# Optimization experiments

Measured on AMD Instinct MI355X. Metric: run time of the kernel, lower is better.

The kernel has to match this reference:

```python
import jax, jax.numpy as jnp
import numpy as np

RADII = (0.8, 1.6)
NSAMPLES = (16, 32)
NUM_GRIDPOINTS = 216


def rotate_z(points, theta):
    # points (b, n, m, 3), theta (b, n); rotate xy about z-axis
    c = jnp.cos(theta)[:, :, None]
    s = jnp.sin(theta)[:, :, None]
    x, y, z = points[..., 0], points[..., 1], points[..., 2]
    return jnp.stack([c * x - s * y, s * x + c * y, z], axis=-1)


def ball_query(d2, radius, nsample):
    # d2: (b, Ng, K) squared distances. Returns first nsample in-radius point
    # indices per query (CUDA ball_query semantics: pad with first found index,
    # 0 if none found).
    K = d2.shape[-1]
    ar = jnp.arange(K, dtype=jnp.int32)
    scores = jnp.where(d2 < radius * radius, ar, K)  # K == sentinel for 'not in ball'
    idx = -jax.lax.top_k(-scores, nsample)[0]        # nsample smallest => first hits, ascending
    first = idx[..., :1]
    idx = jnp.where(idx >= K, first, idx)
    idx = jnp.where(idx >= K, 0, idx)
    return idx


def gather_group(xyz, feats_t, new_xyz, idx):
    # xyz (b,K,3), feats_t (b,K,C), new_xyz (b,Ng,3), idx (b,Ng,ns)
    gx = jax.vmap(lambda p, i: p[i])(xyz, idx)      # (b,Ng,ns,3)
    gf = jax.vmap(lambda f, i: f[i])(feats_t, idx)  # (b,Ng,ns,C)
    rel = gx - new_xyz[:, :, None, :]               # use_xyz=True relative coords
    return jnp.concatenate([rel, gf], axis=-1)      # (b,Ng,ns,3+C)


def setup_inputs() -> dict:
    key = jax.random.key(0)
    ks = jax.random.split(key, 12)
    b, n, m, K, C = 2, 48, NUM_GRIDPOINTS, 2048, 128
    proposals = jax.random.uniform(ks[0], (b, n, 7), dtype=jnp.float32)
    keypoint_xyz = jax.random.normal(ks[1], (b, K, 3), dtype=jnp.float32)
    keypoint_features = jax.random.normal(ks[2], (b, C, K), dtype=jnp.float32)
    grid_noise = jax.random.uniform(ks[3], (b, n, m, 3), dtype=jnp.float32)

    def lin(k, o, i):
        return jax.random.normal(k, (o, i), dtype=jnp.float32) / np.float32(np.sqrt(i))

    w0_0 = lin(ks[4], 64, C + 3)
    w0_1 = lin(ks[5], 64, 64)
    w1_0 = lin(ks[6], 64, C + 3)
    w1_1 = lin(ks[7], 64, 64)
    red_w0 = lin(ks[8], 256, 128 * m)
    red_w1 = lin(ks[9], 256, 256)
    z64 = jnp.zeros((64,), jnp.float32)
    return {
        'proposals': proposals, 'keypoint_xyz': keypoint_xyz,
        'keypoint_features': keypoint_features, 'grid_noise': grid_noise,
        'w0_0': w0_0, 'b0_0': z64, 'w0_1': w0_1, 'b0_1': z64,
        'w1_0': w1_0, 'b1_0': z64, 'w1_1': w1_1, 'b1_1': z64,
        'red_w0': red_w0, 'red_b0': jnp.zeros((256,), jnp.float32),
        'red_w1': red_w1, 'red_b1': jnp.zeros((256,), jnp.float32),
    }


def reference(proposals, keypoint_xyz, keypoint_features, grid_noise,
              w0_0, b0_0, w0_1, b0_1, w1_0, b1_0, w1_1, b1_1,
              red_w0, red_b0, red_w1, red_b1):
    b, n, _ = proposals.shape
    m = NUM_GRIDPOINTS
    # sample_gridpoints: uniform in box dims, rotate by yaw, shift to center
    grid = grid_noise * proposals[:, :, None, 3:6]
    grid = rotate_z(grid, proposals[..., 6]) + proposals[:, :, None, 0:3]
    new_xyz = grid.reshape(b, n * m, 3)                      # (b, Ng, 3)
    # squared pairwise distances via |a|^2 + |b|^2 - 2ab (avoids (b,Ng,K,3) temp)
    d2 = (jnp.sum(new_xyz * new_xyz, -1)[:, :, None]
          + jnp.sum(keypoint_xyz * keypoint_xyz, -1)[:, None, :]
          - 2.0 * jnp.einsum('bnd,bkd->bnk', new_xyz, keypoint_xyz))
    feats_t = jnp.transpose(keypoint_features, (0, 2, 1))    # (b, K, C)
    scale_params = [((w0_0, b0_0), (w0_1, b0_1)), ((w1_0, b1_0), (w1_1, b1_1))]
    outs = []
    for radius, ns, layers in zip(RADII, NSAMPLES, scale_params):
        idx = ball_query(d2, radius, ns)                     # (b, Ng, ns)
        x = gather_group(keypoint_xyz, feats_t, new_xyz, idx)  # (b, Ng, ns, 3+C)
        for W, bias in layers:                               # shared 1x1-conv MLP (BN folded)
            x = jax.nn.relu(jnp.einsum('bnsc,oc->bnso', x, W) + bias)
        outs.append(jnp.max(x, axis=2))                      # max-pool over neighbors
    x = jnp.concatenate(outs, axis=-1)                       # (b, Ng, Cout)
    Cout = x.shape[-1]
    # (b, Cout, n, m).permute(0,2,1,3).view(b, n, Cout*m) equivalent
    x = x.reshape(b, n, m, Cout).transpose(0, 1, 3, 2).reshape(b, n, Cout * m)
    x = jax.nn.relu(x @ red_w0.T + red_b0)
    x = jax.nn.relu(x @ red_w1.T + red_b1)
    return x
```

## Files before the change

### kernel.cpp

```cpp
#include <hip/hip_runtime.h>
#include <cstdint>

#define NPROP  48
#define MGRID  216
#define NPT    (NPROP*MGRID)
#define KPT    2048
#define CFEAT  128
#define R0SQ   0.64f
#define R1SQ   2.56f
#define NS0    16
#define NS1    32
#define KRED   (CFEAT*MGRID)
#define NPOINTS (2*NPT)
#define NKSPLIT 108

typedef float f32x4  __attribute__((ext_vector_type(4)));
typedef short bf16x8 __attribute__((ext_vector_type(8)));
typedef unsigned long long ull;

#define AFRAG_OFF 0
#define KX4_OFF   8192
#define Q0_OFF    24576
#define POOL_OFF  548864
#define PT_OFF    3203072
#define PART_OFF  5857280

__device__ __forceinline__ unsigned short bf_rne(float x) {
    unsigned u = __float_as_uint(x);
    return (unsigned short)((u + 0x7fffu + ((u >> 16) & 1u)) >> 16);
}
__device__ __forceinline__ float bf_f32(unsigned short h) {
    return __uint_as_float(((unsigned)h) << 16);
}

__global__ __launch_bounds__(64) void k_pre(
    const float* __restrict__ kxyz,
    const float* __restrict__ w01, const float* __restrict__ w11,
    float* __restrict__ ws)
{
    int bid = blockIdx.x;
    if (bid < 16) {
        int kc = bid & 1, ot = (bid >> 1) & 3, s = bid >> 3;
        const float* W = s ? w11 : w01;
        int l   = threadIdx.x;
        int row = ot*16 + (l & 15);
        int k0  = kc*32 + (l >> 4)*8;
        union { unsigned short u16[8]; bf16x8 v; } hh, hl;
#pragma unroll
        for (int j = 0; j < 8; ++j) {
            float x  = W[row*64 + k0 + j];
            unsigned short hi = bf_rne(x);
            hh.u16[j] = hi;
            hl.u16[j] = bf_rne(x - bf_f32(hi));
        }
        bf16x8* Ahi = (bf16x8*)(ws + AFRAG_OFF);
        bf16x8* Alo = Ahi + 16*64;
        int fi = (s*4 + ot)*2 + kc;
        Ahi[fi*64 + l] = hh.v;
        Alo[fi*64 + l] = hl.v;
    } else {
        int idx = (bid - 16)*64 + threadIdx.x;
        const float* kp = kxyz + (size_t)idx*3;
        float kx = kp[0], ky = kp[1], kz = kp[2];
        float kn2 = fmaf(kz, kz, fmaf(ky, ky, kx*kx));
        f32x4 v = {kx, ky, kz, kn2};
        ((f32x4*)(ws + KX4_OFF))[idx] = v;
    }
}

__global__ __launch_bounds__(256) void k_qproj(
    const float* __restrict__ kxyz, const float* __restrict__ feats,
    const float* __restrict__ w0, const float* __restrict__ b0,
    const float* __restrict__ w1, const float* __restrict__ b1,
    float* __restrict__ ws)
{
    __shared__ float wl[64*131];
    int bid  = blockIdx.x;
    int kgrp = bid & 511;
    int s    = (bid >> 9) & 1;
    int b    = bid >> 10;
    const float* W    = s ? w1 : w0;
    const float* bias = s ? b1 : b0;
    for (int i = threadIdx.x; i < 64*131; i += 256) wl[i] = W[i];
    __syncthreads();
    int k = kgrp*4 + (threadIdx.x >> 6);
    int o = threadIdx.x & 63;
    float acc = bias[o];
    const float* kp = kxyz + ((size_t)b*KPT + k)*3;
    acc = fmaf(wl[o*131+0], kp[0], acc);
    acc = fmaf(wl[o*131+1], kp[1], acc);
    acc = fmaf(wl[o*131+2], kp[2], acc);
    const float* f = feats + (size_t)b*CFEAT*KPT + k;
#pragma unroll 8
    for (int c = 0; c < CFEAT; ++c)
        acc = fmaf(wl[o*131+3+c], f[(size_t)c*KPT], acc);
    ws[Q0_OFF + (size_t)s*(2*KPT*64) + ((size_t)b*KPT + k)*64 + o] = acc;
}

template <int NST>
__device__ __forceinline__ void build_bfrag(
    const float* __restrict__ Qb, const int* __restrict__ idxl,
    const float* __restrict__ u_lds,
    bf16x8 (&Bhi)[NST][2], bf16x8 (&Blo)[NST][2], int lane)
{
    const int g = lane >> 4;
#pragma unroll
    for (int st = 0; st < NST; ++st) {
        int sp = idxl[st*16 + (lane & 15)];
        const float* qr = Qb + ((size_t)sp << 6) + g*8;
#pragma unroll
        for (int kc = 0; kc < 2; ++kc) {
            f32x4 q0 = *(const f32x4*)(qr + kc*32);
            f32x4 q1 = *(const f32x4*)(qr + kc*32 + 4);
            f32x4 u0 = *(const f32x4*)(u_lds + kc*32 + g*8);
            f32x4 u1 = *(const f32x4*)(u_lds + kc*32 + g*8 + 4);
            union { unsigned short u16[8]; bf16x8 v; } hh, hl;
#pragma unroll
            for (int j = 0; j < 4; ++j) {
                float x = fmaxf(q0[j] - u0[j], 0.f);
                unsigned short hi = bf_rne(x);
                hh.u16[j] = hi;
                hl.u16[j] = bf_rne(x - bf_f32(hi));
                float y = fmaxf(q1[j] - u1[j], 0.f);
                unsigned short hi2 = bf_rne(y);
                hh.u16[j+4] = hi2;
                hl.u16[j+4] = bf_rne(y - bf_f32(hi2));
            }
            Bhi[st][kc] = hh.v;
            Blo[st][kc] = hl.v;
        }
    }
}

template <int NST>
__device__ __forceinline__ void mfma_eval(
    const bf16x8* Ahi, const bf16x8* Alo,
    const float* __restrict__ bs,
    const bf16x8 (&Bhi)[NST][2], const bf16x8 (&Blo)[NST][2],
    float* stage, int sbase, int lane)
{
    const int g = lane >> 4;
#pragma unroll
    for (int ot = 0; ot < 4; ++ot) {
        int fi = (sbase + ot)*2;
        bf16x8 ah0 = Ahi[(fi+0)*64 + lane];
        bf16x8 ah1 = Ahi[(fi+1)*64 + lane];
        bf16x8 al0 = Alo[(fi+0)*64 + lane];
        bf16x8 al1 = Alo[(fi+1)*64 + lane];
        f32x4 bv = *(const f32x4*)(bs + ot*16 + g*4);
        f32x4 rmax = {0.f, 0.f, 0.f, 0.f};
#pragma unroll
        for (int st = 0; st < NST; ++st) {
            f32x4 acc = {0.f, 0.f, 0.f, 0.f};
            acc = __builtin_amdgcn_mfma_f32_16x16x32_bf16(al0, Bhi[st][0], acc, 0,0,0);
            acc = __builtin_amdgcn_mfma_f32_16x16x32_bf16(al1, Bhi[st][1], acc, 0,0,0);
            acc = __builtin_amdgcn_mfma_f32_16x16x32_bf16(ah0, Blo[st][0], acc, 0,0,0);
            acc = __builtin_amdgcn_mfma_f32_16x16x32_bf16(ah1, Blo[st][1], acc, 0,0,0);
            acc = __builtin_amdgcn_mfma_f32_16x16x32_bf16(ah0, Bhi[st][0], acc, 0,0,0);
            acc = __builtin_amdgcn_mfma_f32_16x16x32_bf16(ah1, Bhi[st][1], acc, 0,0,0);
#pragma unroll
            for (int r = 0; r < 4; ++r)
                rmax[r] = fmaxf(rmax[r], fmaxf(acc[r] + bv[r], 0.f));
        }
#pragma unroll
        for (int m = 1; m < 16; m <<= 1) {
#pragma unroll
            for (int r = 0; r < 4; ++r)
                rmax[r] = fmaxf(rmax[r], __shfl_xor(rmax[r], m));
        }
        if ((lane & 15) == 0)
            *(f32x4*)(stage + ot*16 + g*4) = rmax;
    }
}

__global__ __launch_bounds__(256) void k_main(
    const float* __restrict__ proposals, const float* __restrict__ grid_noise,
    const float* __restrict__ w00, const float* __restrict__ b01,
    const float* __restrict__ w10, const float* __restrict__ b11,
    float* __restrict__ ws)
{
    __shared__ __align__(16) float afrag[8192];
    __shared__ int idx0s[4][NS0];
    __shared__ int idx1s[4][NS1];
    __shared__ __align__(16) float u0l[4][64], u1l[4][64];
    __shared__ __align__(16) float stage[4][64];
    const int wid  = threadIdx.x >> 6;
    const int lane = threadIdx.x & 63;

    {
        const f32x4* src = (const f32x4*)(ws + AFRAG_OFF);
        f32x4* dst = (f32x4*)afrag;
        for (int t = threadIdx.x; t < 2048; t += 256) dst[t] = src[t];
    }
    __syncthreads();

    const int p = blockIdx.x*4 + wid;
    int b   = p / NPT;
    int rem = p - b*NPT;
    int i   = rem / MGRID;
    int g   = rem - i*MGRID;

    float a0x = w00[lane*131+0], a0y = w00[lane*131+1], a0z = w00[lane*131+2];
    float a1x = w10[lane*131+0], a1y = w10[lane*131+1], a1z = w10[lane*131+2];

    const float* pr = proposals  + ((size_t)b*NPROP + i)*7;
    const float* gn = grid_noise + (((size_t)b*NPROP + i)*MGRID + g)*3;
    float gx = gn[0]*pr[3], gy = gn[1]*pr[4], gz = gn[2]*pr[5];
    float th = pr[6];
    float ss = sinf(th), cc = cosf(th);
    float nx = cc*gx - ss*gy + pr[0];
    float ny = ss*gx + cc*gy + pr[1];
    float nz = gz + pr[2];
    float pn2 = nx*nx + ny*ny + nz*nz;
    u0l[wid][lane] = a0x*nx + a0y*ny + a0z*nz;
    u1l[wid][lane] = a1x*nx + a1y*ny + a1z*nz;

    int* idx0 = idx0s[wid];
    int* idx1 = idx1s[wid];
    int cnt0 = 0, cnt1 = 0;
    const f32x4* kx4 = (const f32x4*)(ws + KX4_OFF) + (size_t)b*KPT;
    ull ltm = (1ull << lane) - 1ull;

#define BQ_PROC(D2, RSQ, KK, CNT, IDX, NSV)                                   \
    {                                                                         \
        ull m = __ballot((D2) < RSQ);                                         \
        if (m) {                                                              \
            int pre = __popcll(m & ltm);                                      \
            if (((m >> lane) & 1ull) && CNT + pre < NSV) IDX[CNT + pre] = (KK);\
            CNT += __popcll(m);                                               \
        }                                                                     \
    }

    for (int ck = 0; ck < KPT/64; ck += 2) {
        f32x4 ka  = kx4[ck*64 + lane];
        f32x4 kc2 = kx4[ck*64 + 64 + lane];
        float dta = fmaf(nz, ka.z, fmaf(ny, ka.y, nx*ka.x));
        float d2a = fmaf(-2.f, dta, pn2 + ka.w);
        float dtb = fmaf(nz, kc2.z, fmaf(ny, kc2.y, nx*kc2.x));
        float d2b = fmaf(-2.f, dtb, pn2 + kc2.w);
        int kka = ck*64 + lane, kkb = kka + 64;
        if (cnt0 < NS0) {
            BQ_PROC(d2a, R0SQ, kka, cnt0, idx0, NS0)
            BQ_PROC(d2b, R0SQ, kkb, cnt0, idx0, NS0)
        }
        if (cnt1 < NS1) {
            BQ_PROC(d2a, R1SQ, kka, cnt1, idx1, NS1)
            BQ_PROC(d2b, R1SQ, kkb, cnt1, idx1, NS1)
        }
        if (cnt0 >= NS0 && cnt1 >= NS1) break;
    }
#undef BQ_PROC

    if (lane == 0) {
        if (cnt0 == 0) idx0[0] = 0;
        if (cnt1 == 0) idx1[0] = 0;
    }
    asm volatile("s_waitcnt lgkmcnt(0)" ::: "memory");
    __builtin_amdgcn_wave_barrier();
    int na0 = cnt0 ? min(cnt0, NS0) : 1;
    int na1 = cnt1 ? min(cnt1, NS1) : 1;
    int f0 = idx0[0], f1 = idx1[0];
    if (lane >= na0 && lane < NS0) idx0[lane] = f0;
    if (lane >= na1 && lane < NS1) idx1[lane] = f1;
    asm volatile("s_waitcnt lgkmcnt(0)" ::: "memory");
    __builtin_amdgcn_wave_barrier();

    const float*  Qb0 = ws + Q0_OFF + (size_t)b*(KPT*64);
    const float*  Qb1 = ws + Q0_OFF + (size_t)(2*KPT*64) + (size_t)b*(KPT*64);
    const bf16x8* Ahi = (const bf16x8*)afrag;
    const bf16x8* Alo = Ahi + 16*64;

    bf16x8 B0hi[1][2], B0lo[1][2], B1hi[2][2], B1lo[2][2];
    build_bfrag<1>(Qb0, idx0, u0l[wid], B0hi, B0lo, lane);
    build_bfrag<2>(Qb1, idx1, u1l[wid], B1hi, B1lo, lane);

    mfma_eval<1>(Ahi, Alo, b01, B0hi, B0lo, stage[wid], 0, lane);
    asm volatile("s_waitcnt lgkmcnt(0)" ::: "memory");
    __builtin_amdgcn_wave_barrier();
    float mx0 = stage[wid][lane];
    __builtin_amdgcn_wave_barrier();

    mfma_eval<2>(Ahi, Alo, b11, B1hi, B1lo, stage[wid], 4, lane);
    asm volatile("s_waitcnt lgkmcnt(0)" ::: "memory");
    __builtin_amdgcn_wave_barrier();
    float mx1 = stage[wid][lane];

    ws[POOL_OFF + (size_t)p*CFEAT + lane]      = mx0;
    ws[POOL_OFF + (size_t)p*CFEAT + 64 + lane] = mx1;
}

template <int W>
__device__ __forceinline__ void ptr_tile(const float* __restrict__ in,
                                         float* __restrict__ out,
                                         float* __restrict__ t, int g0)
{
    for (int idx = threadIdx.x; idx < 128*W; idx += 256) {
        int gg = idx >> 7, c = idx & 127;
        t[c*(W+1) + gg] = in[(size_t)(g0+gg)*128 + c];
    }
    __syncthreads();
    for (int idx = threadIdx.x; idx < 128*W; idx += 256) {
        int c = idx / W, gg = idx - c*W;
        out[c*216 + g0 + gg] = t[c*(W+1) + gg];
    }
}

__global__ __launch_bounds__(256) void k_ptr(float* __restrict__ ws)
{
    __shared__ float t[128*33];
    int bid = blockIdx.x;
    int row = bid / 7, tt = bid - row*7;
    const float* in = ws + POOL_OFF + (size_t)row*MGRID*CFEAT;
    float* out = ws + PT_OFF + (size_t)row*KRED;
    if (tt < 6) ptr_tile<32>(in, out, t, tt*32);
    else        ptr_tile<24>(in, out, t, 192);
}

__global__ __launch_bounds__(256) void k_red0(
    const float* __restrict__ A, const float* __restrict__ w0,
    float* __restrict__ part)
{
    __shared__ __align__(16) float Al[96*68];
    __shared__ __align__(16) float Bl[64*68];
    int bid = blockIdx.x;
    int ot  = bid & 3;
    int ks  = bid >> 2;
    int tid = threadIdx.x;
    int tx  = tid & 15, ty = tid >> 4;
    float acc[6][4] = {};

    for (int chunk = 0; chunk < 4; ++chunk) {
        int kk0 = ks*256 + chunk*64;
#pragma unroll
        for (int j = 0; j < 6; ++j) {
            int f4i = tid + j*256;
            int rr = f4i >> 4, c4 = f4i & 15;
            float4 v = *(const float4*)(A + (size_t)rr*KRED + kk0 + c4*4);
            *(float4*)(Al + rr*68 + c4*4) = v;
        }
#pragma unroll
        for (int j = 0; j < 4; ++j) {
            int f4i = tid + j*256;
            int rr = f4i >> 4, c4 = f4i & 15;
            float4 v = *(const float4*)(w0 + (size_t)(ot*64+rr)*KRED + kk0 + c4*4);
            *(float4*)(Bl + rr*68 + c4*4) = v;
        }
        __syncthreads();
#pragma unroll
        for (int k4 = 0; k4 < 16; ++k4) {
            float4 av[6], bv[4];
#pragma unroll
            for (int q = 0; q < 6; ++q) av[q] = *(const float4*)(Al + (ty*6+q)*68 + k4*4);
#pragma unroll
            for (int u = 0; u < 4; ++u) bv[u] = *(const float4*)(Bl + (u*16+tx)*68 + k4*4);
#pragma unroll
            for (int q = 0; q < 6; ++q)
#pragma unroll
                for (int u = 0; u < 4; ++u) {
                    acc[q][u] = fmaf(av[q].x, bv[u].x, acc[q][u]);
                    acc[q][u] = fmaf(av[q].y, bv[u].y, acc[q][u]);
                    acc[q][u] = fmaf(av[q].z, bv[u].z, acc[q][u]);
                    acc[q][u] = fmaf(av[q].w, bv[u].w, acc[q][u]);
                }
        }
        __syncthreads();
    }
    float* pp = part + (size_t)ks*(96*256);
#pragma unroll
    for (int q = 0; q < 6; ++q)
#pragma unroll
        for (int u = 0; u < 4; ++u)
            pp[(size_t)(ty*6+q)*256 + ot*64 + u*16 + tx] = acc[q][u];
}

__global__ __launch_bounds__(256) void k_fin(
    const float* __restrict__ part, const float* __restrict__ rb0,
    const float* __restrict__ w1, const float* __restrict__ rb1,
    float* __restrict__ out)
{
    __shared__ __align__(16) float hbuf[256];
    int r = blockIdx.x, o = threadIdx.x;
    const float* pp = part + (size_t)r*256 + o;
    float s0 = 0.f, s1 = 0.f, s2 = 0.f, s3 = 0.f;
#pragma unroll 4
    for (int ks = 0; ks < NKSPLIT; ks += 4) {
        s0 += pp[(size_t)(ks+0)*(96*256)];
        s1 += pp[(size_t)(ks+1)*(96*256)];
        s2 += pp[(size_t)(ks+2)*(96*256)];
        s3 += pp[(size_t)(ks+3)*(96*256)];
    }
    float h = fmaxf(((s0 + s1) + (s2 + s3)) + rb0[o], 0.f);
    hbuf[o] = h;
    __syncthreads();
    float a0 = rb1[o], a1 = 0.f, a2 = 0.f, a3 = 0.f;
    const float4* wrow = (const float4*)(w1 + (size_t)o*256);
    const float4* hv   = (const float4*)hbuf;
#pragma unroll 8
    for (int j = 0; j < 64; ++j) {
        float4 w = wrow[j], x = hv[j];
        a0 = fmaf(w.x, x.x, a0);
        a1 = fmaf(w.y, x.y, a1);
        a2 = fmaf(w.z, x.z, a2);
        a3 = fmaf(w.w, x.w, a3);
    }
    out[(size_t)r*256 + o] = fmaxf((a0 + a1) + (a2 + a3), 0.f);
}

extern "C" void kernel_launch(void* const* d_in, const int* in_sizes, int n_in,
                              void* d_out, int out_size, void* d_ws, size_t ws_size,
                              hipStream_t stream)
{
    (void)in_sizes; (void)n_in; (void)out_size; (void)ws_size;
    const float* proposals = (const float*)d_in[0];
    const float* kxyz      = (const float*)d_in[1];
    const float* feats     = (const float*)d_in[2];
    const float* gnoise    = (const float*)d_in[3];
    const float* w0_0 = (const float*)d_in[4];
    const float* b0_0 = (const float*)d_in[5];
    const float* w0_1 = (const float*)d_in[6];
    const float* b0_1 = (const float*)d_in[7];
    const float* w1_0 = (const float*)d_in[8];
    const float* b1_0 = (const float*)d_in[9];
    const float* w1_1 = (const float*)d_in[10];
    const float* b1_1 = (const float*)d_in[11];
    const float* rw0  = (const float*)d_in[12];
    const float* rb0  = (const float*)d_in[13];
    const float* rw1  = (const float*)d_in[14];
    const float* rb1  = (const float*)d_in[15];
    float* ws  = (float*)d_ws;
    float* out = (float*)d_out;

    k_pre  <<<  80,  64, 0, stream>>>(kxyz, w0_1, w1_1, ws);
    k_qproj<<<2048, 256, 0, stream>>>(kxyz, feats, w0_0, b0_0, w1_0, b1_0, ws);
    k_main <<<5184, 256, 0, stream>>>(proposals, gnoise,
                                      w0_0, b0_1, w1_0, b1_1, ws);
    k_ptr  <<< 672, 256, 0, stream>>>(ws);
    k_red0 <<< 432, 256, 0, stream>>>(ws + PT_OFF, rw0, ws + PART_OFF);
    k_fin  <<<  96, 256, 0, stream>>>(ws + PART_OFF, rb0, rw1, rb1, out);
}
```

Before: 247.6 us.

## Transpose MFMA operands in k_main to pool in registers and double block size

Swaps the MFMA operand roles so the gathered hidden activations form the row operand and the weights the column operand. The max-pool over neighbors then needs only two cross-lane shuffles per output tile, and the result is chosen per lane with selects instead of a 16-lane shuffle tree plus an LDS staging round-trip. k_main also moves to 512-thread blocks (8 waves, launch bounds 512,6), so the weight-fragment LDS copy is amortised over twice as many points. The larger blocks and the occupancy hint may raise register pressure or limit occupancy.

```diff
diff --git a/kernel.cpp b/kernel.cpp
--- a/kernel.cpp
+++ b/kernel.cpp
@@ -53,11 +53,11 @@
             hh.u16[j] = hi;
             hl.u16[j] = bf_rne(x - bf_f32(hi));
         }
-        bf16x8* Ahi = (bf16x8*)(ws + AFRAG_OFF);
-        bf16x8* Alo = Ahi + 16*64;
+        bf16x8* Whi = (bf16x8*)(ws + AFRAG_OFF);
+        bf16x8* Wlo = Whi + 16*64;
         int fi = (s*4 + ot)*2 + kc;
-        Ahi[fi*64 + l] = hh.v;
-        Alo[fi*64 + l] = hl.v;
+        Whi[fi*64 + l] = hh.v;
+        Wlo[fi*64 + l] = hl.v;
     } else {
         int idx = (bid - 16)*64 + threadIdx.x;
         const float* kp = kxyz + (size_t)idx*3;
@@ -98,10 +98,10 @@
 }
 
 template <int NST>
-__device__ __forceinline__ void build_bfrag(
+__device__ __forceinline__ void build_hfrag(
     const float* __restrict__ Qb, const int* __restrict__ idxl,
     const float* __restrict__ u_lds,
-    bf16x8 (&Bhi)[NST][2], bf16x8 (&Blo)[NST][2], int lane)
+    bf16x8 (&Hhi)[NST][2], bf16x8 (&Hlo)[NST][2], int lane)
 {
     const int g = lane >> 4;
 #pragma unroll
@@ -126,75 +126,75 @@
                 hh.u16[j+4] = hi2;
                 hl.u16[j+4] = bf_rne(y - bf_f32(hi2));
             }
-            Bhi[st][kc] = hh.v;
-            Blo[st][kc] = hl.v;
+            Hhi[st][kc] = hh.v;
+            Hlo[st][kc] = hl.v;
         }
     }
 }
 
 template <int NST>
-__device__ __forceinline__ void mfma_eval(
-    const bf16x8* Ahi, const bf16x8* Alo,
+__device__ __forceinline__ float eval_T(
+    const bf16x8* Whi, const bf16x8* Wlo,
     const float* __restrict__ bs,
-    const bf16x8 (&Bhi)[NST][2], const bf16x8 (&Blo)[NST][2],
-    float* stage, int sbase, int lane)
-{
-    const int g = lane >> 4;
-#pragma unroll
-    for (int ot = 0; ot < 4; ++ot) {
-        int fi = (sbase + ot)*2;
-        bf16x8 ah0 = Ahi[(fi+0)*64 + lane];
-        bf16x8 ah1 = Ahi[(fi+1)*64 + lane];
-        bf16x8 al0 = Alo[(fi+0)*64 + lane];
-        bf16x8 al1 = Alo[(fi+1)*64 + lane];
-        f32x4 bv = *(const f32x4*)(bs + ot*16 + g*4);
-        f32x4 rmax = {0.f, 0.f, 0.f, 0.f};
-#pragma unroll
-        for (int st = 0; st < NST; ++st) {
-            f32x4 acc = {0.f, 0.f, 0.f, 0.f};
-            acc = __builtin_amdgcn_mfma_f32_16x16x32_bf16(al0, Bhi[st][0], acc, 0,0,0);
-            acc = __builtin_amdgcn_mfma_f32_16x16x32_bf16(al1, Bhi[st][1], acc, 0,0,0);
-            acc = __builtin_amdgcn_mfma_f32_16x16x32_bf16(ah0, Blo[st][0], acc, 0,0,0);
-            acc = __builtin_amdgcn_mfma_f32_16x16x32_bf16(ah1, Blo[st][1], acc, 0,0,0);
-            acc = __builtin_amdgcn_mfma_f32_16x16x32_bf16(ah0, Bhi[st][0], acc, 0,0,0);
-            acc = __builtin_amdgcn_mfma_f32_16x16x32_bf16(ah1, Bhi[st][1], acc, 0,0,0);
-#pragma unroll
-            for (int r = 0; r < 4; ++r)
-                rmax[r] = fmaxf(rmax[r], fmaxf(acc[r] + bv[r], 0.f));
-        }
-#pragma unroll
-        for (int m = 1; m < 16; m <<= 1) {
-#pragma unroll
-            for (int r = 0; r < 4; ++r)
-                rmax[r] = fmaxf(rmax[r], __shfl_xor(rmax[r], m));
-        }
-        if ((lane & 15) == 0)
-            *(f32x4*)(stage + ot*16 + g*4) = rmax;
-    }
-}
-
-__global__ __launch_bounds__(256) void k_main(
+    const bf16x8 (&Hhi)[NST][2], const bf16x8 (&Hlo)[NST][2],
+    int sbase, int lane)
+{
+    float r0, r1, r2, r3;
+#define EVAL_OT(OT, ROUT)                                                     \
+    {                                                                         \
+        int fi = (sbase + (OT))*2;                                            \
+        bf16x8 wh0 = Whi[(fi+0)*64 + lane];                                   \
+        bf16x8 wh1 = Whi[(fi+1)*64 + lane];                                   \
+        bf16x8 wl0 = Wlo[(fi+0)*64 + lane];                                   \
+        bf16x8 wl1 = Wlo[(fi+1)*64 + lane];                                   \
+        float bc = bs[(OT)*16 + (lane & 15)];                                 \
+        f32x4 rmax = {0.f, 0.f, 0.f, 0.f};                                    \
+        _Pragma("unroll")                                                     \
+        for (int st = 0; st < NST; ++st) {                                    \
+            f32x4 acc = {0.f, 0.f, 0.f, 0.f};                                 \
+            acc = __builtin_amdgcn_mfma_f32_16x16x32_bf16(Hlo[st][0], wh0, acc, 0,0,0); \
+            acc = __builtin_amdgcn_mfma_f32_16x16x32_bf16(Hlo[st][1], wh1, acc, 0,0,0); \
+            acc = __builtin_amdgcn_mfma_f32_16x16x32_bf16(Hhi[st][0], wl0, acc, 0,0,0); \
+            acc = __builtin_amdgcn_mfma_f32_16x16x32_bf16(Hhi[st][1], wl1, acc, 0,0,0); \
+            acc = __builtin_amdgcn_mfma_f32_16x16x32_bf16(Hhi[st][0], wh0, acc, 0,0,0); \
+            acc = __builtin_amdgcn_mfma_f32_16x16x32_bf16(Hhi[st][1], wh1, acc, 0,0,0); \
+            _Pragma("unroll")                                                 \
+            for (int r = 0; r < 4; ++r)                                       \
+                rmax[r] = fmaxf(rmax[r], fmaxf(acc[r] + bc, 0.f));            \
+        }                                                                     \
+        float mm = fmaxf(fmaxf(rmax[0], rmax[1]), fmaxf(rmax[2], rmax[3]));   \
+        mm = fmaxf(mm, __shfl_xor(mm, 16));                                   \
+        mm = fmaxf(mm, __shfl_xor(mm, 32));                                   \
+        ROUT = mm;                                                            \
+    }
+    EVAL_OT(0, r0) EVAL_OT(1, r1) EVAL_OT(2, r2) EVAL_OT(3, r3)
+#undef EVAL_OT
+    float v01 = (lane & 16) ? r1 : r0;
+    float v23 = (lane & 16) ? r3 : r2;
+    return (lane & 32) ? v23 : v01;
+}
+
+__global__ __launch_bounds__(512, 6) void k_main(
     const float* __restrict__ proposals, const float* __restrict__ grid_noise,
     const float* __restrict__ w00, const float* __restrict__ b01,
     const float* __restrict__ w10, const float* __restrict__ b11,
     float* __restrict__ ws)
 {
     __shared__ __align__(16) float afrag[8192];
-    __shared__ int idx0s[4][NS0];
-    __shared__ int idx1s[4][NS1];
-    __shared__ __align__(16) float u0l[4][64], u1l[4][64];
-    __shared__ __align__(16) float stage[4][64];
+    __shared__ int idx0s[8][NS0];
+    __shared__ int idx1s[8][NS1];
+    __shared__ __align__(16) float u0l[8][64], u1l[8][64];
     const int wid  = threadIdx.x >> 6;
     const int lane = threadIdx.x & 63;
 
     {
         const f32x4* src = (const f32x4*)(ws + AFRAG_OFF);
         f32x4* dst = (f32x4*)afrag;
-        for (int t = threadIdx.x; t < 2048; t += 256) dst[t] = src[t];
+        for (int t = threadIdx.x; t < 2048; t += 512) dst[t] = src[t];
     }
     __syncthreads();
 
-    const int p = blockIdx.x*4 + wid;
+    const int p = blockIdx.x*8 + wid;
     int b   = p / NPT;
     int rem = p - b*NPT;
     int i   = rem / MGRID;
@@ -267,23 +267,15 @@
 
     const float*  Qb0 = ws + Q0_OFF + (size_t)b*(KPT*64);
     const float*  Qb1 = ws + Q0_OFF + (size_t)(2*KPT*64) + (size_t)b*(KPT*64);
-    const bf16x8* Ahi = (const bf16x8*)afrag;
-    const bf16x8* Alo = Ahi + 16*64;
-
-    bf16x8 B0hi[1][2], B0lo[1][2], B1hi[2][2], B1lo[2][2];
-    build_bfrag<1>(Qb0, idx0, u0l[wid], B0hi, B0lo, lane);
-    build_bfrag<2>(Qb1, idx1, u1l[wid], B1hi, B1lo, lane);
-
-    mfma_eval<1>(Ahi, Alo, b01, B0hi, B0lo, stage[wid], 0, lane);
-    asm volatile("s_waitcnt lgkmcnt(0)" ::: "memory");
-    __builtin_amdgcn_wave_barrier();
-    float mx0 = stage[wid][lane];
-    __builtin_amdgcn_wave_barrier();
-
-    mfma_eval<2>(Ahi, Alo, b11, B1hi, B1lo, stage[wid], 4, lane);
-    asm volatile("s_waitcnt lgkmcnt(0)" ::: "memory");
-    __builtin_amdgcn_wave_barrier();
-    float mx1 = stage[wid][lane];
+    const bf16x8* Whi = (const bf16x8*)afrag;
+    const bf16x8* Wlo = Whi + 16*64;
+
+    bf16x8 H0hi[1][2], H0lo[1][2], H1hi[2][2], H1lo[2][2];
+    build_hfrag<1>(Qb0, idx0, u0l[wid], H0hi, H0lo, lane);
+    build_hfrag<2>(Qb1, idx1, u1l[wid], H1hi, H1lo, lane);
+
+    float mx0 = eval_T<1>(Whi, Wlo, b01, H0hi, H0lo, 0, lane);
+    float mx1 = eval_T<2>(Whi, Wlo, b11, H1hi, H1lo, 4, lane);
 
     ws[POOL_OFF + (size_t)p*CFEAT + lane]      = mx0;
     ws[POOL_OFF + (size_t)p*CFEAT + 64 + lane] = mx1;
@@ -432,7 +424,7 @@
 
     k_pre  <<<  80,  64, 0, stream>>>(kxyz, w0_1, w1_1, ws);
     k_qproj<<<2048, 256, 0, stream>>>(kxyz, feats, w0_0, b0_0, w1_0, b1_0, ws);
-    k_main <<<5184, 256, 0, stream>>>(proposals, gnoise,
+    k_main <<<2592, 512, 0, stream>>>(proposals, gnoise,
                                       w0_0, b0_1, w1_0, b1_1, ws);
     k_ptr  <<< 672, 256, 0, stream>>>(ws);
     k_red0 <<< 432, 256, 0, stream>>>(ws + PT_OFF, rw0, ws + PART_OFF);
```

Measured after the change: 274.7 us. +10.9%, slower.
